# Performance work log

Hardware: AMD Instinct MI355X
Metric: run time of the kernel (lower is better)

Reference implementation:

```python
import jax, jax.numpy as jnp
import numpy as np
from math import sqrt

KERNEL = 25
INV_SQRT2 = 1.0 / sqrt(2.0)


def _moving_avg(xt):
    # xt: [B, L]; replicate-pad then average-pool k=25 stride=1 -> [B, L]
    pad_l = (KERNEL - 1) // 2
    pad_r = KERNEL - 1 - pad_l
    xp = jnp.pad(xt, ((0, 0), (pad_l, pad_r)), mode='edge')[:, None, :]  # [B,1,Lp]
    k = jnp.full((1, 1, KERNEL), 1.0 / KERNEL, dtype=xt.dtype)  # [O,I,W]
    out = jax.lax.conv_general_dilated(xp, k, window_strides=(1,), padding='VALID',
                                       dimension_numbers=('NCH', 'OIH', 'NCH'))
    return out[:, 0, :]


def setup_inputs() -> dict:
    key = jax.random.key(0)
    ks = jax.random.split(key, 7)
    B, L, P, H = 8192, 4096, 720, 2048
    return {
        'x': jax.random.normal(ks[0], (B, L, 1), dtype=jnp.float32),
        'W_trend': jax.random.normal(ks[1], (P, L), dtype=jnp.float32) * 0.02,
        'b_trend': jax.random.normal(ks[2], (P,), dtype=jnp.float32) * 0.02,
        'W_lo': jax.random.normal(ks[3], (P, H), dtype=jnp.float32) * 0.02,
        'b_lo': jax.random.normal(ks[4], (P,), dtype=jnp.float32) * 0.02,
        'W_hi': jax.random.normal(ks[5], (P, H), dtype=jnp.float32) * 0.02,
        'b_hi': jax.random.normal(ks[6], (P,), dtype=jnp.float32) * 0.02,
    }


def reference(x, W_trend, b_trend, W_lo, b_lo, W_hi, b_hi):
    xt = x[..., 0]                              # [B, L]
    trend = _moving_avg(xt)                     # [B, L]
    res = xt - trend                            # [B, L]
    res_mean = jnp.mean(res, axis=-1, keepdims=True)
    # torch.std is unbiased (ddof=1)
    res_std = jnp.std(res, axis=-1, keepdims=True, ddof=1) + 1e-5
    res_norm = (res - res_mean) / res_std       # [B, L]
    # Haar DWT (stride-2 conv with [1,1]/sqrt2 and [1,-1]/sqrt2); L even -> no pad
    even, odd = res_norm[:, 0::2], res_norm[:, 1::2]  # [B, L/2]
    res_lo = (even + odd) * INV_SQRT2
    res_hi = (even - odd) * INV_SQRT2
    pred_trend = trend @ W_trend.T + b_trend    # [B, P]
    pred_res = (res_lo @ W_lo.T + b_lo) + (res_hi @ W_hi.T + b_hi)
    total = pred_trend + pred_res * res_std     # res_std broadcasts [B,1]
    return total[..., None]                     # [B, P, 1]
```

## Files before the change

kernel.cpp:

```cpp
#include <hip/hip_runtime.h>

typedef unsigned short u16;
typedef unsigned int   u32;
typedef __attribute__((ext_vector_type(8))) short bf16x8;
typedef __attribute__((ext_vector_type(4))) float f32x4;

#define LROW 4096
#define NB   8192
#define PCOL 720
#define NPAD 768
#define HH   2048
#define INV_SQRT2F 0.70710678118654752440f

#define WS_XBF_BYTES ((size_t)67108864)
#define WS_G_BYTES   ((size_t)6291456)
#define WS_MIN       (WS_XBF_BYTES + WS_G_BYTES + (size_t)NB * 4)

__device__ __forceinline__ u16 f2bf(float f) {
    union { float f; u32 u; } v; v.f = f;
    u32 r = v.u + 0x7FFFu + ((v.u >> 16) & 1u);
    return (u16)(r >> 16);
}

#define SWZ(i) ((i) ^ (((i) >> 5) & 31))

__global__ __launch_bounds__(256) void prep_rows(const float* __restrict__ x,
                                                 u16* __restrict__ xbf,
                                                 float* __restrict__ stdv) {
    __shared__ float S[LROW];
    __shared__ float wred[4];
    __shared__ float ends[2];
    __shared__ float rred[8];
    const int tid = threadIdx.x;
    const int lane = tid & 63, wv = tid >> 6;
    const size_t b = blockIdx.x;

    const float4* xr4 = (const float4*)(x + b * LROW);
    float4 q0 = xr4[tid * 4 + 0], q1 = xr4[tid * 4 + 1];
    float4 q2 = xr4[tid * 4 + 2], q3 = xr4[tid * 4 + 3];
    float r[16];
    r[0]=q0.x; r[1]=q0.y; r[2]=q0.z; r[3]=q0.w;
    r[4]=q1.x; r[5]=q1.y; r[6]=q1.z; r[7]=q1.w;
    r[8]=q2.x; r[9]=q2.y; r[10]=q2.z; r[11]=q2.w;
    r[12]=q3.x; r[13]=q3.y; r[14]=q3.z; r[15]=q3.w;

    float ps[16];
    float a = 0.f;
    #pragma unroll
    for (int k = 0; k < 16; ++k) { a += r[k]; ps[k] = a; }
    const float segsum = a;

    float v = segsum;
    #pragma unroll
    for (int off = 1; off < 64; off <<= 1) {
        float o = __shfl_up(v, off);
        if (lane >= off) v += o;
    }
    if (lane == 63) wred[wv] = v;
    if (tid == 0)   ends[0] = r[0];
    if (tid == 255) ends[1] = r[15];
    __syncthreads();

    float wbase = 0.f;
    #pragma unroll
    for (int w = 0; w < 4; ++w) if (w < wv) wbase += wred[w];
    const float ebase = wbase + v - segsum;

    #pragma unroll
    for (int k = 0; k < 16; ++k) {
        const int i = (tid << 4) + k;
        S[SWZ(i)] = ebase + ps[k];
    }
    __syncthreads();

    const float x0 = ends[0], xl = ends[1];
    float s1 = 0.f, s2 = 0.f;
    u16 ob[16];
    #pragma unroll
    for (int k = 0; k < 16; ++k) {
        const int i = (tid << 4) + k;
        int h = i + 12; h = h > LROW - 1 ? LROW - 1 : h;
        float wsum = S[SWZ(h)];
        if (i >= 13) wsum -= S[SWZ(i - 13)];
        if (i < 12) wsum += (float)(12 - i) * x0;
        if (i > LROW - 13) wsum += (float)(i - (LROW - 13)) * xl;
        const float xi = r[k];
        const float rr = xi - wsum * 0.04f;
        s1 += rr; s2 += rr * rr;
        ob[k] = f2bf(xi);
    }

    uint4 o0, o1;
    o0.x = (u32)ob[0]  | ((u32)ob[1]  << 16);
    o0.y = (u32)ob[2]  | ((u32)ob[3]  << 16);
    o0.z = (u32)ob[4]  | ((u32)ob[5]  << 16);
    o0.w = (u32)ob[6]  | ((u32)ob[7]  << 16);
    o1.x = (u32)ob[8]  | ((u32)ob[9]  << 16);
    o1.y = (u32)ob[10] | ((u32)ob[11] << 16);
    o1.z = (u32)ob[12] | ((u32)ob[13] << 16);
    o1.w = (u32)ob[14] | ((u32)ob[15] << 16);
    uint4* op = (uint4*)(xbf + b * LROW + ((size_t)tid << 4));
    op[0] = o0; op[1] = o1;

    #pragma unroll
    for (int off = 32; off; off >>= 1) {
        s1 += __shfl_down(s1, off);
        s2 += __shfl_down(s2, off);
    }
    if (lane == 0) { rred[wv * 2] = s1; rred[wv * 2 + 1] = s2; }
    __syncthreads();
    if (tid == 0) {
        const float S1 = rred[0] + rred[2] + rred[4] + rred[6];
        const float S2 = rred[1] + rred[3] + rred[5] + rred[7];
        const float mean = S1 / (float)LROW;
        float var = (S2 - (float)LROW * mean * mean) / (float)(LROW - 1);
        var = var < 0.f ? 0.f : var;
        stdv[b] = sqrtf(var) + 1e-5f;
    }
}

__global__ __launch_bounds__(256) void prep_weights(const float* __restrict__ Wt,
                                                    const float* __restrict__ Wlo,
                                                    const float* __restrict__ Whi,
                                                    u16* __restrict__ Gm) {
    __shared__ float S[LROW];
    __shared__ float wred[4];
    __shared__ float sred[4];
    const int tid = threadIdx.x;
    const int lane = tid & 63, wv = tid >> 6;
    const int p = blockIdx.x;
    u16* grow = Gm + (size_t)p * LROW;
    if (p >= PCOL) {
        uint4 z; z.x = z.y = z.z = z.w = 0u;
        uint4* g4 = (uint4*)grow;
        for (int i = tid; i < LROW / 8; i += 256) g4[i] = z;
        return;
    }
    const float4* wt4 = (const float4*)(Wt + (size_t)p * LROW);
    float4 q0 = wt4[tid * 4 + 0], q1 = wt4[tid * 4 + 1];
    float4 q2 = wt4[tid * 4 + 2], q3 = wt4[tid * 4 + 3];
    const float4* lo4 = (const float4*)(Wlo + (size_t)p * HH);
    const float4* hi4 = (const float4*)(Whi + (size_t)p * HH);
    float4 a0 = lo4[tid * 2 + 0], a1 = lo4[tid * 2 + 1];
    float4 b0 = hi4[tid * 2 + 0], b1 = hi4[tid * 2 + 1];

    float w[16];
    w[0]=q0.x; w[1]=q0.y; w[2]=q0.z; w[3]=q0.w;
    w[4]=q1.x; w[5]=q1.y; w[6]=q1.z; w[7]=q1.w;
    w[8]=q2.x; w[9]=q2.y; w[10]=q2.z; w[11]=q2.w;
    w[12]=q3.x; w[13]=q3.y; w[14]=q3.z; w[15]=q3.w;
    float lv[8] = {a0.x,a0.y,a0.z,a0.w,a1.x,a1.y,a1.z,a1.w};
    float hv[8] = {b0.x,b0.y,b0.z,b0.w,b1.x,b1.y,b1.z,b1.w};

    float u[16], z_[16];
    float slo = 0.f;
    #pragma unroll
    for (int j = 0; j < 8; ++j) {
        u[2*j]   = (lv[j] + hv[j]) * INV_SQRT2F;
        u[2*j+1] = (lv[j] - hv[j]) * INV_SQRT2F;
        slo += lv[j];
    }
    #pragma unroll
    for (int k = 0; k < 16; ++k) z_[k] = w[k] - u[k];

    float ps[16];
    float a = 0.f;
    #pragma unroll
    for (int k = 0; k < 16; ++k) { a += z_[k]; ps[k] = a; }
    const float segsum = a;

    float v = segsum;
    #pragma unroll
    for (int off = 1; off < 64; off <<= 1) {
        float o = __shfl_up(v, off);
        if (lane >= off) v += o;
    }
    if (lane == 63) wred[wv] = v;
    #pragma unroll
    for (int off = 32; off; off >>= 1) slo += __shfl_down(slo, off);
    if (lane == 0) sred[wv] = slo;
    __syncthreads();

    float wbase = 0.f;
    #pragma unroll
    for (int ww = 0; ww < 4; ++ww) if (ww < wv) wbase += wred[ww];
    const float ebase = wbase + v - segsum;
    const float SLO = sred[0] + sred[1] + sred[2] + sred[3];

    #pragma unroll
    for (int k = 0; k < 16; ++k) {
        const int i = (tid << 4) + k;
        S[SWZ(i)] = ebase + ps[k];
    }
    __syncthreads();

    const float coef = -1.4142135623730951f * SLO / (float)LROW;
    u16 ob[16];
    #pragma unroll
    for (int k = 0; k < 16; ++k) {
        const int l = (tid << 4) + k;
        float zT;
        if (l == 0) {
            float acc = 0.f;
            for (int m = 0; m <= 12; ++m) acc += S[SWZ(m)];
            zT = acc * 0.04f;
        } else if (l == LROW - 1) {
            float acc = 0.f;
            for (int m = 0; m <= 12; ++m) acc += S[SWZ(LROW - 2 - m)];
            zT = (13.f * S[SWZ(LROW - 1)] - acc) * 0.04f;
        } else {
            int h = l + 12; h = h > LROW - 1 ? LROW - 1 : h;
            float t_ = S[SWZ(h)];
            if (l >= 13) t_ -= S[SWZ(l - 13)];
            zT = t_ * 0.04f;
        }
        float c;
        const int dmin = l < (LROW - 1 - l) ? l : (LROW - 1 - l);
        if (dmin >= 12)      c = 0.f;
        else if (dmin == 0)  c = -66.f / 25.f;
        else                 c = (float)(12 - dmin) * 0.04f;
        ob[k] = f2bf(zT + u[k] + coef * c);
    }

    uint4 o0, o1;
    o0.x = (u32)ob[0]  | ((u32)ob[1]  << 16);
    o0.y = (u32)ob[2]  | ((u32)ob[3]  << 16);
    o0.z = (u32)ob[4]  | ((u32)ob[5]  << 16);
    o0.w = (u32)ob[6]  | ((u32)ob[7]  << 16);
    o1.x = (u32)ob[8]  | ((u32)ob[9]  << 16);
    o1.y = (u32)ob[10] | ((u32)ob[11] << 16);
    o1.z = (u32)ob[12] | ((u32)ob[13] << 16);
    o1.w = (u32)ob[14] | ((u32)ob[15] << 16);
    uint4* op = (uint4*)(grow + ((size_t)tid << 4));
    op[0] = o0; op[1] = o1;
}

typedef __attribute__((address_space(1))) void gvoid;
typedef __attribute__((address_space(3))) void lvoid;
#define GLD16(g, l_) __builtin_amdgcn_global_load_lds((gvoid*)(g), (lvoid*)(l_), 16, 0, 0)
#define MF(a, b, c) __builtin_amdgcn_mfma_f32_16x16x32_bf16(a, b, c, 0, 0, 0)

#define ABUFB 16384
#define BBASE 32768
#define BBUFB 12288

#define STAGE_AB(T, DB) do { \
    char* da_ = Sm + (DB) * ABUFB + wid * 4096; \
    char* db_ = Sm + BBASE + (DB) * BBUFB + wid * 3072; \
    const size_t go_ = (size_t)(T) * 128; \
    GLD16(sA0 + go_, da_); \
    GLD16(sA0 + go_ + 65536, da_ + 1024); \
    GLD16(sA0 + go_ + 131072, da_ + 2048); \
    GLD16(sA0 + go_ + 196608, da_ + 3072); \
    GLD16(sB0 + go_, db_); \
    GLD16(sB0 + go_ + 65536, db_ + 1024); \
    GLD16(sB0 + go_ + 131072, db_ + 2048); \
} while (0)

#define READ_FRAGS(P, BUF) do { \
    const char* a_ = Sm + (BUF) * ABUFB + aro; \
    const char* b_ = Sm + BBASE + (BUF) * BBUFB + bro; \
    P##A0 = *(const bf16x8*)(a_); \
    P##A1 = *(const bf16x8*)(a_ + 2048); \
    P##A2 = *(const bf16x8*)(a_ + 4096); \
    P##A3 = *(const bf16x8*)(a_ + 6144); \
    P##B0 = *(const bf16x8*)(b_); \
    P##B1 = *(const bf16x8*)(b_ + 2048); \
    P##B2 = *(const bf16x8*)(b_ + 4096); \
    P##B3 = *(const bf16x8*)(b_ + 6144); \
    P##B4 = *(const bf16x8*)(b_ + 8192); \
    P##B5 = *(const bf16x8*)(b_ + 10240); \
} while (0)

#define MFMA24(P) do { \
    acc[0][0]=MF(P##A0,P##B0,acc[0][0]); acc[0][1]=MF(P##A0,P##B1,acc[0][1]); acc[0][2]=MF(P##A0,P##B2,acc[0][2]); \
    acc[0][3]=MF(P##A0,P##B3,acc[0][3]); acc[0][4]=MF(P##A0,P##B4,acc[0][4]); acc[0][5]=MF(P##A0,P##B5,acc[0][5]); \
    acc[1][0]=MF(P##A1,P##B0,acc[1][0]); acc[1][1]=MF(P##A1,P##B1,acc[1][1]); acc[1][2]=MF(P##A1,P##B2,acc[1][2]); \
    acc[1][3]=MF(P##A1,P##B3,acc[1][3]); acc[1][4]=MF(P##A1,P##B4,acc[1][4]); acc[1][5]=MF(P##A1,P##B5,acc[1][5]); \
    acc[2][0]=MF(P##A2,P##B0,acc[2][0]); acc[2][1]=MF(P##A2,P##B1,acc[2][1]); acc[2][2]=MF(P##A2,P##B2,acc[2][2]); \
    acc[2][3]=MF(P##A2,P##B3,acc[2][3]); acc[2][4]=MF(P##A2,P##B4,acc[2][4]); acc[2][5]=MF(P##A2,P##B5,acc[2][5]); \
    acc[3][0]=MF(P##A3,P##B0,acc[3][0]); acc[3][1]=MF(P##A3,P##B1,acc[3][1]); acc[3][2]=MF(P##A3,P##B2,acc[3][2]); \
    acc[3][3]=MF(P##A3,P##B3,acc[3][3]); acc[3][4]=MF(P##A3,P##B4,acc[3][4]); acc[3][5]=MF(P##A3,P##B5,acc[3][5]); \
} while (0)

#define ITER(T, CUR, NXT, DOSTAGE, DOREAD) do { \
    asm volatile("s_waitcnt vmcnt(0) lgkmcnt(0)" ::: "memory"); \
    __builtin_amdgcn_s_barrier(); \
    __builtin_amdgcn_sched_barrier(0); \
    if (DOSTAGE) STAGE_AB((T) + 2, (T) & 1); \
    if (DOREAD) READ_FRAGS(NXT, ((T) + 1) & 1); \
    __builtin_amdgcn_sched_barrier(0); \
    __builtin_amdgcn_s_setprio(1); \
    MFMA24(CUR); \
    __builtin_amdgcn_s_setprio(0); \
} while (0)

__global__ __launch_bounds__(256, 2) void gemm_fused(const u16* __restrict__ Abf,
                                                     const u16* __restrict__ Gbf,
                                                     const float* __restrict__ bt,
                                                     const float* __restrict__ bl,
                                                     const float* __restrict__ bh,
                                                     const float* __restrict__ stdv,
                                                     float* __restrict__ out) {
    __shared__ __align__(16) char Sm[57344];
    const int tid = threadIdx.x;
    const int l = tid & 63, wid = tid >> 6;
    const int wm = wid & 1, kp = wid >> 1;

    const int orig = blockIdx.x;
    const int chunk = orig & 7, pos = orig >> 3;
    const int bx = pos & 7;
    const int by = (chunk << 3) + (pos >> 3);
    const int m0 = by * 128;
    const int n0 = bx * 96;

    const int sgb = (((l & 7) ^ (l >> 3)) << 4);
    const char* sA0 = (const char*)Abf + ((size_t)(m0 + wid * 32 + (l >> 3)) << 13) + sgb;
    const char* sB0 = (const char*)Gbf + ((size_t)(n0 + wid * 24 + (l >> 3)) << 13) + sgb;

    const int slot16 = ((((kp << 2) + (l >> 4)) ^ (l & 7)) << 4);
    const int aro = (wm * 64 + (l & 15)) * 128 + slot16;
    const int bro = (l & 15) * 128 + slot16;

    f32x4 acc[4][6] = {};
    bf16x8 XA0, XA1, XA2, XA3, XB0, XB1, XB2, XB3, XB4, XB5;
    bf16x8 YA0, YA1, YA2, YA3, YB0, YB1, YB2, YB3, YB4, YB5;

    STAGE_AB(0, 0);
    STAGE_AB(1, 1);
    asm volatile("s_waitcnt vmcnt(7)" ::: "memory");
    __builtin_amdgcn_s_barrier();
    __builtin_amdgcn_sched_barrier(0);
    READ_FRAGS(X, 0);

    for (int t = 0; t < 60; t += 2) {
        ITER(t,     X, Y, 1, 1);
        ITER(t + 1, Y, X, 1, 1);
    }
    ITER(60, X, Y, 1, 1);
    ITER(61, Y, X, 1, 1);
    ITER(62, X, Y, 0, 1);
    ITER(63, Y, X, 0, 0);

    __syncthreads();
    float* red = (float*)Sm;
    const int rr = (l >> 4) << 2;
    const int cc = l & 15;
    const int rbase = wm * 6528;
    if (kp == 1) {
        #pragma unroll
        for (int m = 0; m < 4; ++m)
            #pragma unroll
            for (int n = 0; n < 6; ++n)
                *(f32x4*)(red + rbase + (n * 16 + cc) * 68 + m * 16 + rr) = acc[m][n];
    }
    __syncthreads();
    if (kp == 0) {
        const int crow = m0 + wm * 64 + rr;
        const int ccol = n0 + cc;
        float btv[6], bsv[6];
        #pragma unroll
        for (int n = 0; n < 6; ++n) {
            const int col = ccol + n * 16;
            if (col < PCOL) { btv[n] = bt[col]; bsv[n] = bl[col] + bh[col]; }
            else            { btv[n] = 0.f; bsv[n] = 0.f; }
        }
        #pragma unroll
        for (int m = 0; m < 4; ++m) {
            const int row = crow + m * 16;
            const float4 sv = *(const float4*)(stdv + row);
            #pragma unroll
            for (int n = 0; n < 6; ++n) {
                const int col = ccol + n * 16;
                if (col < PCOL) {
                    const f32x4 pv = *(const f32x4*)(red + rbase + (n * 16 + cc) * 68 + m * 16 + rr);
                    float* orow = out + (size_t)row * PCOL + col;
                    #pragma unroll
                    for (int j = 0; j < 4; ++j) {
                        const float s = (j == 0) ? sv.x : (j == 1) ? sv.y : (j == 2) ? sv.z : sv.w;
                        orow[(size_t)j * PCOL] = acc[m][n][j] + pv[j] + btv[n] + s * bsv[n];
                    }
                }
            }
        }
    }
}

extern "C" void kernel_launch(void* const* d_in, const int* in_sizes, int n_in,
                              void* d_out, int out_size, void* d_ws, size_t ws_size,
                              hipStream_t stream) {
    (void)in_sizes; (void)n_in; (void)out_size;
    if (ws_size < WS_MIN) return;

    const float* x  = (const float*)d_in[0];
    const float* Wt = (const float*)d_in[1];
    const float* bt = (const float*)d_in[2];
    const float* Wl = (const float*)d_in[3];
    const float* bl = (const float*)d_in[4];
    const float* Wh = (const float*)d_in[5];
    const float* bh = (const float*)d_in[6];
    float* out = (float*)d_out;

    char* ws = (char*)d_ws;
    u16*   xbf = (u16*)ws;
    u16*   Gm  = (u16*)(ws + WS_XBF_BYTES);
    float* sd  = (float*)(ws + WS_XBF_BYTES + WS_G_BYTES);

    prep_rows<<<NB, 256, 0, stream>>>(x, xbf, sd);
    prep_weights<<<NPAD, 256, 0, stream>>>(Wt, Wl, Wh, Gm);
    gemm_fused<<<512, 256, 0, stream>>>(xbf, Gm, bt, bl, bh, sd, out);
}
```

Baseline: 95.39 us.

## Load A fragments directly from global to registers, triple-buffer B in LDS

The A operand is no longer staged through LDS. Each wave loads its A fragments straight from global memory into registers one k-step ahead, while B moves to a three-deep LDS ring buffer staged three steps ahead, with partial vmcnt waits. The aim is to cut LDS traffic and capacity pressure and to deepen prefetch for B. The cost is that the direct A loads are per-lane 16-byte reads spread across rows, so coalescing is poorer, and the vmcnt counting becomes fragile because A and B loads now share the same counter.

```diff
diff --git a/kernel.cpp b/kernel.cpp
--- a/kernel.cpp
+++ b/kernel.cpp
@@ -240,58 +240,55 @@
 #define GLD16(g, l_) __builtin_amdgcn_global_load_lds((gvoid*)(g), (lvoid*)(l_), 16, 0, 0)
 #define MF(a, b, c) __builtin_amdgcn_mfma_f32_16x16x32_bf16(a, b, c, 0, 0, 0)
 
-#define ABUFB 16384
-#define BBASE 32768
 #define BBUFB 12288
 
-#define STAGE_AB(T, DB) do { \
-    char* da_ = Sm + (DB) * ABUFB + wid * 4096; \
-    char* db_ = Sm + BBASE + (DB) * BBUFB + wid * 3072; \
+#define STAGE_B(T, DB) do { \
+    char* db_ = Sm + (DB) * BBUFB + wid * 3072; \
     const size_t go_ = (size_t)(T) * 128; \
-    GLD16(sA0 + go_, da_); \
-    GLD16(sA0 + go_ + 65536, da_ + 1024); \
-    GLD16(sA0 + go_ + 131072, da_ + 2048); \
-    GLD16(sA0 + go_ + 196608, da_ + 3072); \
-    GLD16(sB0 + go_, db_); \
-    GLD16(sB0 + go_ + 65536, db_ + 1024); \
+    GLD16(sB0 + go_,          db_); \
+    GLD16(sB0 + go_ + 65536,  db_ + 1024); \
     GLD16(sB0 + go_ + 131072, db_ + 2048); \
 } while (0)
 
-#define READ_FRAGS(P, BUF) do { \
-    const char* a_ = Sm + (BUF) * ABUFB + aro; \
-    const char* b_ = Sm + BBASE + (BUF) * BBUFB + bro; \
-    P##A0 = *(const bf16x8*)(a_); \
-    P##A1 = *(const bf16x8*)(a_ + 2048); \
-    P##A2 = *(const bf16x8*)(a_ + 4096); \
-    P##A3 = *(const bf16x8*)(a_ + 6144); \
-    P##B0 = *(const bf16x8*)(b_); \
-    P##B1 = *(const bf16x8*)(b_ + 2048); \
-    P##B2 = *(const bf16x8*)(b_ + 4096); \
-    P##B3 = *(const bf16x8*)(b_ + 6144); \
-    P##B4 = *(const bf16x8*)(b_ + 8192); \
-    P##B5 = *(const bf16x8*)(b_ + 10240); \
+#define LOAD_A(T, P) do { \
+    const char* s_ = pa + (size_t)(T) * 128; \
+    P##0 = *(const bf16x8*)(s_); \
+    P##1 = *(const bf16x8*)(s_ + 131072); \
+    P##2 = *(const bf16x8*)(s_ + 262144); \
+    P##3 = *(const bf16x8*)(s_ + 393216); \
 } while (0)
 
-#define MFMA24(P) do { \
-    acc[0][0]=MF(P##A0,P##B0,acc[0][0]); acc[0][1]=MF(P##A0,P##B1,acc[0][1]); acc[0][2]=MF(P##A0,P##B2,acc[0][2]); \
-    acc[0][3]=MF(P##A0,P##B3,acc[0][3]); acc[0][4]=MF(P##A0,P##B4,acc[0][4]); acc[0][5]=MF(P##A0,P##B5,acc[0][5]); \
-    acc[1][0]=MF(P##A1,P##B0,acc[1][0]); acc[1][1]=MF(P##A1,P##B1,acc[1][1]); acc[1][2]=MF(P##A1,P##B2,acc[1][2]); \
-    acc[1][3]=MF(P##A1,P##B3,acc[1][3]); acc[1][4]=MF(P##A1,P##B4,acc[1][4]); acc[1][5]=MF(P##A1,P##B5,acc[1][5]); \
-    acc[2][0]=MF(P##A2,P##B0,acc[2][0]); acc[2][1]=MF(P##A2,P##B1,acc[2][1]); acc[2][2]=MF(P##A2,P##B2,acc[2][2]); \
-    acc[2][3]=MF(P##A2,P##B3,acc[2][3]); acc[2][4]=MF(P##A2,P##B4,acc[2][4]); acc[2][5]=MF(P##A2,P##B5,acc[2][5]); \
-    acc[3][0]=MF(P##A3,P##B0,acc[3][0]); acc[3][1]=MF(P##A3,P##B1,acc[3][1]); acc[3][2]=MF(P##A3,P##B2,acc[3][2]); \
-    acc[3][3]=MF(P##A3,P##B3,acc[3][3]); acc[3][4]=MF(P##A3,P##B4,acc[3][4]); acc[3][5]=MF(P##A3,P##B5,acc[3][5]); \
+#define READ_B(P, DB) do { \
+    const char* b_ = Sm + (DB) * BBUFB + bro; \
+    P##0 = *(const bf16x8*)(b_); \
+    P##1 = *(const bf16x8*)(b_ + 2048); \
+    P##2 = *(const bf16x8*)(b_ + 4096); \
+    P##3 = *(const bf16x8*)(b_ + 6144); \
+    P##4 = *(const bf16x8*)(b_ + 8192); \
+    P##5 = *(const bf16x8*)(b_ + 10240); \
 } while (0)
 
-#define ITER(T, CUR, NXT, DOSTAGE, DOREAD) do { \
-    asm volatile("s_waitcnt vmcnt(0) lgkmcnt(0)" ::: "memory"); \
+#define MFMA24(AP, BP) do { \
+    acc[0][0]=MF(AP##0,BP##0,acc[0][0]); acc[0][1]=MF(AP##0,BP##1,acc[0][1]); acc[0][2]=MF(AP##0,BP##2,acc[0][2]); \
+    acc[0][3]=MF(AP##0,BP##3,acc[0][3]); acc[0][4]=MF(AP##0,BP##4,acc[0][4]); acc[0][5]=MF(AP##0,BP##5,acc[0][5]); \
+    acc[1][0]=MF(AP##1,BP##0,acc[1][0]); acc[1][1]=MF(AP##1,BP##1,acc[1][1]); acc[1][2]=MF(AP##1,BP##2,acc[1][2]); \
+    acc[1][3]=MF(AP##1,BP##3,acc[1][3]); acc[1][4]=MF(AP##1,BP##4,acc[1][4]); acc[1][5]=MF(AP##1,BP##5,acc[1][5]); \
+    acc[2][0]=MF(AP##2,BP##0,acc[2][0]); acc[2][1]=MF(AP##2,BP##1,acc[2][1]); acc[2][2]=MF(AP##2,BP##2,acc[2][2]); \
+    acc[2][3]=MF(AP##2,BP##3,acc[2][3]); acc[2][4]=MF(AP##2,BP##4,acc[2][4]); acc[2][5]=MF(AP##2,BP##5,acc[2][5]); \
+    acc[3][0]=MF(AP##3,BP##0,acc[3][0]); acc[3][1]=MF(AP##3,BP##1,acc[3][1]); acc[3][2]=MF(AP##3,BP##2,acc[3][2]); \
+    acc[3][3]=MF(AP##3,BP##3,acc[3][3]); acc[3][4]=MF(AP##3,BP##4,acc[3][4]); acc[3][5]=MF(AP##3,BP##5,acc[3][5]); \
+} while (0)
+
+#define ITER(T, CA, NA, CB, NB, VM, SBUF, RBUF, DOA, DOSB, DORB) do { \
+    asm volatile("s_waitcnt vmcnt(" #VM ") lgkmcnt(0)" ::: "memory"); \
     __builtin_amdgcn_s_barrier(); \
     __builtin_amdgcn_sched_barrier(0); \
-    if (DOSTAGE) STAGE_AB((T) + 2, (T) & 1); \
-    if (DOREAD) READ_FRAGS(NXT, ((T) + 1) & 1); \
+    if (DOA)  LOAD_A((T) + 1, NA); \
+    if (DOSB) STAGE_B((T) + 3, SBUF); \
+    if (DORB) READ_B(NB, RBUF); \
     __builtin_amdgcn_sched_barrier(0); \
     __builtin_amdgcn_s_setprio(1); \
-    MFMA24(CUR); \
+    MFMA24(CA, CB); \
     __builtin_amdgcn_s_setprio(0); \
 } while (0)
 
@@ -302,7 +299,7 @@
                                                      const float* __restrict__ bh,
                                                      const float* __restrict__ stdv,
                                                      float* __restrict__ out) {
-    __shared__ __align__(16) char Sm[57344];
+    __shared__ __align__(16) char Sm[53248];
     const int tid = threadIdx.x;
     const int l = tid & 63, wid = tid >> 6;
     const int wm = wid & 1, kp = wid >> 1;
@@ -314,33 +311,40 @@
     const int m0 = by * 128;
     const int n0 = bx * 96;
 
+    const char* pa = (const char*)Abf
+        + ((size_t)(m0 + wm * 64 + (l & 15)) << 13) + kp * 64 + ((l >> 4) << 4);
+
     const int sgb = (((l & 7) ^ (l >> 3)) << 4);
-    const char* sA0 = (const char*)Abf + ((size_t)(m0 + wid * 32 + (l >> 3)) << 13) + sgb;
     const char* sB0 = (const char*)Gbf + ((size_t)(n0 + wid * 24 + (l >> 3)) << 13) + sgb;
 
     const int slot16 = ((((kp << 2) + (l >> 4)) ^ (l & 7)) << 4);
-    const int aro = (wm * 64 + (l & 15)) * 128 + slot16;
     const int bro = (l & 15) * 128 + slot16;
 
     f32x4 acc[4][6] = {};
-    bf16x8 XA0, XA1, XA2, XA3, XB0, XB1, XB2, XB3, XB4, XB5;
-    bf16x8 YA0, YA1, YA2, YA3, YB0, YB1, YB2, YB3, YB4, YB5;
-
-    STAGE_AB(0, 0);
-    STAGE_AB(1, 1);
-    asm volatile("s_waitcnt vmcnt(7)" ::: "memory");
+    bf16x8 XA0, XA1, XA2, XA3, YA0, YA1, YA2, YA3;
+    bf16x8 XB0, XB1, XB2, XB3, XB4, XB5, YB0, YB1, YB2, YB3, YB4, YB5;
+
+    LOAD_A(0, XA);
+    STAGE_B(0, 0);
+    STAGE_B(1, 1);
+    STAGE_B(2, 2);
+    asm volatile("s_waitcnt vmcnt(6)" ::: "memory");
     __builtin_amdgcn_s_barrier();
     __builtin_amdgcn_sched_barrier(0);
-    READ_FRAGS(X, 0);
-
-    for (int t = 0; t < 60; t += 2) {
-        ITER(t,     X, Y, 1, 1);
-        ITER(t + 1, Y, X, 1, 1);
-    }
-    ITER(60, X, Y, 1, 1);
-    ITER(61, Y, X, 1, 1);
-    ITER(62, X, Y, 0, 1);
-    ITER(63, Y, X, 0, 0);
+    READ_B(XB, 0);
+
+    for (int t = 0; t < 60; t += 6) {
+        ITER(t + 0, XA, YA, XB, YB, 3, 0, 1, 1, 1, 1);
+        ITER(t + 1, YA, XA, YB, XB, 3, 1, 2, 1, 1, 1);
+        ITER(t + 2, XA, YA, XB, YB, 3, 2, 0, 1, 1, 1);
+        ITER(t + 3, YA, XA, YB, XB, 3, 0, 1, 1, 1, 1);
+        ITER(t + 4, XA, YA, XB, YB, 3, 1, 2, 1, 1, 1);
+        ITER(t + 5, YA, XA, YB, XB, 3, 2, 0, 1, 1, 1);
+    }
+    ITER(60, XA, YA, XB, YB, 3, 0, 1, 1, 1, 1);
+    ITER(61, YA, XA, YB, XB, 3, 0, 2, 1, 0, 1);
+    ITER(62, XA, YA, XB, YB, 0, 0, 0, 1, 0, 1);
+    ITER(63, YA, XA, YB, XB, 0, 0, 0, 0, 0, 0);
 
     __syncthreads();
     float* red = (float*)Sm;
```

New measurement: 121.1 us. 1.27x slower.

## Triple-buffer A tiles and split A/B staging with partial vmcnt waits

Applied to the files above, without the earlier changes.

Splits global-to-LDS staging into separate A and B loads. The A operand now gets a three-deep ring buffer prefetched three tiles ahead, while B stays double-buffered two ahead. Each iteration waits on vmcnt(4) instead of draining all outstanding loads, so the newest A loads stay in flight across the barrier. LDS use grows from 56 KB to 72 KB per block, which may constrain the two-blocks-per-CU occupancy, and the hand-computed buffer rotation and wait counts are fragile.

```diff
diff --git a/kernel.cpp b/kernel.cpp
--- a/kernel.cpp
+++ b/kernel.cpp
@@ -241,25 +241,29 @@
 #define MF(a, b, c) __builtin_amdgcn_mfma_f32_16x16x32_bf16(a, b, c, 0, 0, 0)
 
 #define ABUFB 16384
-#define BBASE 32768
+#define BBASE 49152
 #define BBUFB 12288
 
-#define STAGE_AB(T, DB) do { \
+#define STAGE_A(T, DB) do { \
     char* da_ = Sm + (DB) * ABUFB + wid * 4096; \
+    const size_t go_ = (size_t)(T) * 128; \
+    GLD16(sA0 + go_,          da_); \
+    GLD16(sA0 + go_ + 65536,  da_ + 1024); \
+    GLD16(sA0 + go_ + 131072, da_ + 2048); \
+    GLD16(sA0 + go_ + 196608, da_ + 3072); \
+} while (0)
+
+#define STAGE_B(T, DB) do { \
     char* db_ = Sm + BBASE + (DB) * BBUFB + wid * 3072; \
     const size_t go_ = (size_t)(T) * 128; \
-    GLD16(sA0 + go_, da_); \
-    GLD16(sA0 + go_ + 65536, da_ + 1024); \
-    GLD16(sA0 + go_ + 131072, da_ + 2048); \
-    GLD16(sA0 + go_ + 196608, da_ + 3072); \
-    GLD16(sB0 + go_, db_); \
-    GLD16(sB0 + go_ + 65536, db_ + 1024); \
+    GLD16(sB0 + go_,          db_); \
+    GLD16(sB0 + go_ + 65536,  db_ + 1024); \
     GLD16(sB0 + go_ + 131072, db_ + 2048); \
 } while (0)
 
-#define READ_FRAGS(P, BUF) do { \
-    const char* a_ = Sm + (BUF) * ABUFB + aro; \
-    const char* b_ = Sm + BBASE + (BUF) * BBUFB + bro; \
+#define READ_FRAGS(P, AB, BB) do { \
+    const char* a_ = Sm + (AB) * ABUFB + aro; \
+    const char* b_ = Sm + BBASE + (BB) * BBUFB + bro; \
     P##A0 = *(const bf16x8*)(a_); \
     P##A1 = *(const bf16x8*)(a_ + 2048); \
     P##A2 = *(const bf16x8*)(a_ + 4096); \
@@ -283,12 +287,14 @@
     acc[3][3]=MF(P##A3,P##B3,acc[3][3]); acc[3][4]=MF(P##A3,P##B4,acc[3][4]); acc[3][5]=MF(P##A3,P##B5,acc[3][5]); \
 } while (0)
 
-#define ITER(T, CUR, NXT, DOSTAGE, DOREAD) do { \
-    asm volatile("s_waitcnt vmcnt(0) lgkmcnt(0)" ::: "memory"); \
+#define ITER(T, CUR, NXT, BST, AST, ARD, BRD, VM, SB, SA, RD) do { \
+    asm volatile("s_waitcnt vmcnt(" #VM ") lgkmcnt(0)" ::: "memory"); \
     __builtin_amdgcn_s_barrier(); \
     __builtin_amdgcn_sched_barrier(0); \
-    if (DOSTAGE) STAGE_AB((T) + 2, (T) & 1); \
-    if (DOREAD) READ_FRAGS(NXT, ((T) + 1) & 1); \
+    if (SB) STAGE_B((T) + 2, BST); \
+    if (SA) STAGE_A((T) + 3, AST); \
+    __builtin_amdgcn_sched_barrier(0); \
+    if (RD) READ_FRAGS(NXT, ARD, BRD); \
     __builtin_amdgcn_sched_barrier(0); \
     __builtin_amdgcn_s_setprio(1); \
     MFMA24(CUR); \
@@ -302,7 +308,7 @@
                                                      const float* __restrict__ bh,
                                                      const float* __restrict__ stdv,
                                                      float* __restrict__ out) {
-    __shared__ __align__(16) char Sm[57344];
+    __shared__ __align__(16) char Sm[73728];
     const int tid = threadIdx.x;
     const int l = tid & 63, wid = tid >> 6;
     const int wm = wid & 1, kp = wid >> 1;
@@ -326,21 +332,28 @@
     bf16x8 XA0, XA1, XA2, XA3, XB0, XB1, XB2, XB3, XB4, XB5;
     bf16x8 YA0, YA1, YA2, YA3, YB0, YB1, YB2, YB3, YB4, YB5;
 
-    STAGE_AB(0, 0);
-    STAGE_AB(1, 1);
-    asm volatile("s_waitcnt vmcnt(7)" ::: "memory");
+    STAGE_B(0, 0);
+    STAGE_A(0, 0);
+    STAGE_B(1, 1);
+    STAGE_A(1, 1);
+    STAGE_A(2, 2);
+    asm volatile("s_waitcnt vmcnt(11)" ::: "memory");
     __builtin_amdgcn_s_barrier();
     __builtin_amdgcn_sched_barrier(0);
-    READ_FRAGS(X, 0);
-
-    for (int t = 0; t < 60; t += 2) {
-        ITER(t,     X, Y, 1, 1);
-        ITER(t + 1, Y, X, 1, 1);
-    }
-    ITER(60, X, Y, 1, 1);
-    ITER(61, Y, X, 1, 1);
-    ITER(62, X, Y, 0, 1);
-    ITER(63, Y, X, 0, 0);
+    READ_FRAGS(X, 0, 0);
+
+    for (int t = 0; t < 60; t += 6) {
+        ITER(t + 0, X, Y, 0, 0, 1, 1, 4, 1, 1, 1);
+        ITER(t + 1, Y, X, 1, 1, 2, 0, 4, 1, 1, 1);
+        ITER(t + 2, X, Y, 0, 2, 0, 1, 4, 1, 1, 1);
+        ITER(t + 3, Y, X, 1, 0, 1, 0, 4, 1, 1, 1);
+        ITER(t + 4, X, Y, 0, 1, 2, 1, 4, 1, 1, 1);
+        ITER(t + 5, Y, X, 1, 2, 0, 0, 4, 1, 1, 1);
+    }
+    ITER(60, X, Y, 0, 0, 1, 1, 4, 1, 1, 1);
+    ITER(61, Y, X, 1, 0, 2, 0, 4, 1, 0, 1);
+    ITER(62, X, Y, 0, 0, 0, 1, 0, 0, 0, 1);
+    ITER(63, Y, X, 0, 0, 0, 0, 0, 0, 0, 0);
 
     __syncthreads();
     float* red = (float*)Sm;
```

New measurement: 95.87 us. Within noise of the previous version (+0.5%).
